# Kernel optimization log

Measured on AMD Instinct MI355X. Metric: run time of the kernel, lower is better.

## Reference

```python
import jax, jax.numpy as jnp
import numpy as np

N = 50000      # nodes
E = 600000     # edges
D = 128        # num_features == hidden_dim
H = 1          # heads (only runnable config of this module)
C = 128        # per-head channels
L = 2          # num_layers
G = 64         # graphs in batch
NC = 10        # num_classes


def setup_inputs() -> dict:
    key = jax.random.key(0)
    ks = jax.random.split(key, 12)
    s = 1.0 / np.sqrt(D)
    inp = {
        "x": jax.random.normal(ks[0], (N, D), jnp.float32),
        "edge_index": jax.random.randint(ks[1], (2, E), 0, N),
        "batch": jnp.sort(jax.random.randint(ks[2], (N,), 0, G)),
        # per-layer TransformerConv params (stacked over layers)
        "Wq": jax.random.normal(ks[3], (L, D, H * C), jnp.float32) * s,
        "bq": jax.random.normal(ks[4], (L, H * C), jnp.float32) * 0.01,
        "Wk": jax.random.normal(ks[5], (L, D, H * C), jnp.float32) * s,
        "bk": jax.random.normal(ks[6], (L, H * C), jnp.float32) * 0.01,
        "Wv": jax.random.normal(ks[7], (L, D, H * C), jnp.float32) * s,
        "bv": jax.random.normal(ks[8], (L, H * C), jnp.float32) * 0.01,
        "Ws": jax.random.normal(ks[9], (L, D, H * C), jnp.float32) * s,  # lin_skip (root weight)
        "bs": jax.random.normal(ks[10], (L, H * C), jnp.float32) * 0.01,
        "W_fc": jax.random.normal(ks[11], (H * C, NC), jnp.float32) * (1.0 / np.sqrt(H * C)),
        "b_fc": jnp.zeros((NC,), jnp.float32),
    }
    return inp


def _transformer_conv(x, src, dst, wq, bq, wk, bk, wv, bv, ws, bs):
    n = x.shape[0]
    q = (x @ wq + bq).reshape(n, H, C)
    k = (x @ wk + bk).reshape(n, H, C)
    v = (x @ wv + bv).reshape(n, H, C)
    # edge-wise gather: query from dst (x_i), key/value from src (x_j)
    score = (q[dst] * k[src]).sum(-1) / jnp.sqrt(jnp.float32(C))  # [E, H]
    # segment softmax over incoming edges of each dst node
    m = jax.ops.segment_max(score, dst, num_segments=n)           # [N, H]
    ex = jnp.exp(score - m[dst])
    den = jax.ops.segment_sum(ex, dst, num_segments=n)
    alpha = ex / den[dst]                                         # [E, H]
    agg = jax.ops.segment_sum(alpha[..., None] * v[src], dst, num_segments=n)
    return agg.reshape(n, H * C) + x @ ws + bs                    # concat heads + skip


def reference(x, edge_index, batch, Wq, bq, Wk, bk, Wv, bv, Ws, bs, W_fc, b_fc):
    src, dst = edge_index[0], edge_index[1]
    h = x
    for l in range(L):
        h = jax.nn.relu(_transformer_conv(h, src, dst, Wq[l], bq[l], Wk[l], bk[l],
                                          Wv[l], bv[l], Ws[l], bs[l]))
    # global mean pool per graph
    sums = jax.ops.segment_sum(h, batch, num_segments=G)
    cnts = jax.ops.segment_sum(jnp.ones((h.shape[0],), h.dtype), batch, num_segments=G)
    pooled = sums / jnp.maximum(cnts, 1.0)[:, None]
    logits = pooled @ W_fc + b_fc
    return jax.nn.log_softmax(logits, axis=1)
```

## Files before the change

kernel.cpp:

```cpp
#include <hip/hip_runtime.h>
#include <math.h>

#define NN 50000
#define EE 600000
#define DD 128
#define GG 64
#define NCLS 10
#define PCHUNK 128
#define NTILE (NN / 16)
#define NBUK 196
#define BSTRIDE 4096
#define EPB ((EE + 255) / 256)

typedef __attribute__((ext_vector_type(8))) __bf16 bf16x8;
typedef __attribute__((ext_vector_type(8))) unsigned short u16x8;
typedef __attribute__((ext_vector_type(4))) float f32x4;
typedef __attribute__((ext_vector_type(2))) float f32x2;

__device__ __forceinline__ unsigned short f2bf(float f) {
    unsigned int u = __float_as_uint(f);
    u += 0x7fff + ((u >> 16) & 1);
    return (unsigned short)(u >> 16);
}

__device__ __forceinline__ float bf2f(unsigned short h) {
    return __uint_as_float(((unsigned int)h) << 16);
}

__device__ __forceinline__ float lo16(unsigned int u) { return __uint_as_float(u << 16); }
__device__ __forceinline__ float hi16(unsigned int u) { return __uint_as_float(u & 0xffff0000u); }


__global__ __launch_bounds__(256) void prep_kernel(
    const float* __restrict__ wq, const float* __restrict__ wk,
    const float* __restrict__ wv, const float* __restrict__ ws,
    unsigned short* __restrict__ wt,
    int* __restrict__ bucketcnt, float* __restrict__ gsum) {
    int tid = blockIdx.x * 256 + threadIdx.x;
    int TOT = gridDim.x * 256;
    if (tid < 256) bucketcnt[tid] = 0;
    for (int i = tid; i < GG * DD + GG; i += TOT) gsum[i] = 0.f;
    for (int i = tid; i < 2 * 4 * 16384; i += TOT) {
        int k = i & 127;
        int n = (i >> 7) & 127;
        int lm = i >> 14;
        int l = lm >> 2, m = lm & 3;
        const float* w = (m == 0) ? wq : (m == 1) ? wk : (m == 2) ? wv : ws;
        wt[i] = f2bf(w[l * 16384 + k * 128 + n]);
    }
}


__global__ __launch_bounds__(1024) void bucket_kernel(
    const int* __restrict__ src, const int* __restrict__ dst,
    int* __restrict__ bucketcnt, int2* __restrict__ bedge) {
    __shared__ int hist[256];
    __shared__ int base[256];
    int t = threadIdx.x;
    if (t < 256) hist[t] = 0;
    __syncthreads();
    int e0 = blockIdx.x * EPB;
    int eend = min(e0 + EPB, EE);

    int b0 = -1, b1 = -1, b2 = -1;
    int sl0 = 0, sl1 = 0, sl2 = 0;
    int s0 = 0, s1 = 0, s2 = 0, d0 = 0, d1 = 0, d2 = 0;
    int i = e0 + t;
    if (i < eend) { d0 = dst[i]; s0 = src[i]; b0 = d0 >> 8; sl0 = atomicAdd(&hist[b0], 1); }
    i += 1024;
    if (i < eend) { d1 = dst[i]; s1 = src[i]; b1 = d1 >> 8; sl1 = atomicAdd(&hist[b1], 1); }
    i += 1024;
    if (i < eend) { d2 = dst[i]; s2 = src[i]; b2 = d2 >> 8; sl2 = atomicAdd(&hist[b2], 1); }
    __syncthreads();

    if (t < 256) {
        int h = hist[t];
        base[t] = h ? atomicAdd(&bucketcnt[t], h) : 0;
    }
    __syncthreads();

    if (b0 >= 0) bedge[b0 * BSTRIDE + base[b0] + sl0] = make_int2(s0, d0);
    if (b1 >= 0) bedge[b1 * BSTRIDE + base[b1] + sl1] = make_int2(s1, d1);
    if (b2 >= 0) bedge[b2 * BSTRIDE + base[b2] + sl2] = make_int2(s2, d2);
}


__global__ __launch_bounds__(1024) void bsort_kernel(
    const int* __restrict__ bucketcnt, const int2* __restrict__ bedge,
    int* __restrict__ indptr, int* __restrict__ esrc) {
    __shared__ int buf[256];
    __shared__ int cur[256];
    int b = blockIdx.x;
    int t = threadIdx.x;

    if (t < 256) buf[t] = (t < NBUK) ? bucketcnt[t] : 0;
    __syncthreads();
    if (t < 64) {
        int carry = 0;
        #pragma unroll
        for (int c = 0; c < 4; ++c) {
            int v = buf[c * 64 + t];
            int x = v;
            #pragma unroll
            for (int off = 1; off < 64; off <<= 1) {
                int y = __shfl_up(x, off);
                if (t >= off) x += y;
            }
            cur[c * 64 + t] = carry + x - v;
            carry += __shfl(x, 63);
        }
    }
    __syncthreads();
    int count = buf[b];
    int bstart = cur[b];
    int node0 = b << 8;
    int nn = min(256, NN - node0);
    if (b == 0 && t == 0) indptr[NN] = EE;
    __syncthreads();
    if (t < 256) buf[t] = 0;
    __syncthreads();

    const int2* be = bedge + (size_t)b * BSTRIDE;
    for (int i2 = t; i2 < count; i2 += 1024)
        atomicAdd(&buf[be[i2].y - node0], 1);
    __syncthreads();

    if (t < 64) {
        int carry = 0;
        #pragma unroll
        for (int c = 0; c < 4; ++c) {
            int v = buf[c * 64 + t];
            int x = v;
            #pragma unroll
            for (int off = 1; off < 64; off <<= 1) {
                int y = __shfl_up(x, off);
                if (t >= off) x += y;
            }
            cur[c * 64 + t] = carry + x - v;
            carry += __shfl(x, 63);
        }
    }
    __syncthreads();
    if (t < nn) indptr[node0 + t] = bstart + cur[t];
    __syncthreads();

    for (int i2 = t; i2 < count; i2 += 1024) {
        int2 e = be[i2];
        int slot = atomicAdd(&cur[e.y - node0], 1);
        esrc[bstart + slot] = e.x;
    }
}


template <bool IN_BF16>
__global__ __launch_bounds__(256, 4) void gemm_mfma(
    const void* __restrict__ xin,
    const unsigned short* __restrict__ wt,
    const float* __restrict__ bq, const float* __restrict__ bk,
    const float* __restrict__ bv, const float* __restrict__ bs,
    unsigned short* __restrict__ qb, unsigned short* __restrict__ kvb,
    unsigned short* __restrict__ sb) {
    int gw = blockIdx.x * 4 + (threadIdx.x >> 6);
    int lane = threadIdx.x & 63;
    int mat = (gw >> 1) & 3;
    int ch = gw & 1;
    int wseq = gw >> 3;
    int lr = lane & 15, quad = lane >> 4;

    const unsigned short* wm_ = wt + mat * 16384;
    const float* bias = (mat == 0) ? bq : (mat == 1) ? bk : (mat == 2) ? bv : bs;
    unsigned short* outp; int ostride, ooff;
    if (mat == 0)      { outp = qb;  ostride = 128; ooff = 0; }
    else if (mat == 1) { outp = kvb; ostride = 256; ooff = 0; }
    else if (mat == 2) { outp = kvb; ostride = 256; ooff = 128; }
    else               { outp = sb;  ostride = 128; ooff = 0; }

    bf16x8 bfr[4][4];
    #pragma unroll
    for (int ks = 0; ks < 4; ++ks)
        #pragma unroll
        for (int tn = 0; tn < 4; ++tn)
            bfr[ks][tn] = *(const bf16x8*)(wm_ + (ch * 64 + tn * 16 + lr) * 128
                                               + ks * 32 + quad * 8);
    float bcol[4];
    #pragma unroll
    for (int tn = 0; tn < 4; ++tn) bcol[tn] = bias[ch * 64 + tn * 16 + lr];

    for (int tile = wseq; tile < NTILE; tile += 256) {
        int row0 = tile * 16;
        bf16x8 af[4];
        #pragma unroll
        for (int ks = 0; ks < 4; ++ks) {
            if (IN_BF16) {
                af[ks] = *(const bf16x8*)((const unsigned short*)xin
                             + (size_t)(row0 + lr) * DD + ks * 32 + quad * 8);
            } else {
                const float* p = (const float*)xin
                                 + (size_t)(row0 + lr) * DD + ks * 32 + quad * 8;
                float4 f0 = *(const float4*)p;
                float4 f1 = *(const float4*)(p + 4);
                u16x8 a8;
                a8[0] = f2bf(f0.x); a8[1] = f2bf(f0.y); a8[2] = f2bf(f0.z); a8[3] = f2bf(f0.w);
                a8[4] = f2bf(f1.x); a8[5] = f2bf(f1.y); a8[6] = f2bf(f1.z); a8[7] = f2bf(f1.w);
                af[ks] = *(bf16x8*)&a8;
            }
        }

        f32x4 acc[4];
        #pragma unroll
        for (int tn = 0; tn < 4; ++tn) acc[tn] = (f32x4){0.f, 0.f, 0.f, 0.f};
        #pragma unroll
        for (int ks = 0; ks < 4; ++ks)
            #pragma unroll
            for (int tn = 0; tn < 4; ++tn)
                acc[tn] = __builtin_amdgcn_mfma_f32_16x16x32_bf16(
                    af[ks], bfr[ks][tn], acc[tn], 0, 0, 0);

        #pragma unroll
        for (int tn = 0; tn < 4; ++tn) {
            int col = ch * 64 + tn * 16 + lr;
            int nb = row0 + quad * 4;
            #pragma unroll
            for (int r = 0; r < 4; ++r)
                outp[(size_t)(nb + r) * ostride + ooff + col] = f2bf(acc[tn][r] + bcol[tn]);
        }
    }
}


__global__ __launch_bounds__(256) void kv8_kernel(
    const unsigned short* __restrict__ kvb, unsigned char* __restrict__ kv8) {
    int idx = blockIdx.x * 256 + threadIdx.x;
    int node = idx >> 4, j = idx & 15;
    const unsigned short* base = kvb + (size_t)node * 256;
    uint4 kin = *(const uint4*)(base + j * 8);
    uint4 vin = *(const uint4*)(base + 128 + j * 8);
    unsigned int w0 = __builtin_amdgcn_cvt_pk_fp8_f32(lo16(kin.x), hi16(kin.x), 0, false);
    w0 = __builtin_amdgcn_cvt_pk_fp8_f32(lo16(kin.y), hi16(kin.y), w0, true);
    unsigned int w1 = __builtin_amdgcn_cvt_pk_fp8_f32(lo16(kin.z), hi16(kin.z), 0, false);
    w1 = __builtin_amdgcn_cvt_pk_fp8_f32(lo16(kin.w), hi16(kin.w), w1, true);
    unsigned int w2 = __builtin_amdgcn_cvt_pk_fp8_f32(lo16(vin.x), hi16(vin.x), 0, false);
    w2 = __builtin_amdgcn_cvt_pk_fp8_f32(lo16(vin.y), hi16(vin.y), w2, true);
    unsigned int w3 = __builtin_amdgcn_cvt_pk_fp8_f32(lo16(vin.z), hi16(vin.z), 0, false);
    w3 = __builtin_amdgcn_cvt_pk_fp8_f32(lo16(vin.w), hi16(vin.w), w3, true);
    *(uint4*)(kv8 + (size_t)idx * 16) = make_uint4(w0, w1, w2, w3);
}


__global__ __launch_bounds__(256) void attn_kernel(
    const unsigned short* __restrict__ qb, const unsigned char* __restrict__ kv8,
    const unsigned short* __restrict__ sb,
    const int* __restrict__ indptr, const int* __restrict__ esrc,
    unsigned short* __restrict__ hout, int n) {
    int node = (int)((blockIdx.x * blockDim.x + threadIdx.x) >> 6);
    int lane = threadIdx.x & 63;
    if (node >= n) return;
    int g = lane >> 4, j = lane & 15;

    u16x8 q8 = *(const u16x8*)(qb + (size_t)node * DD + j * 8);
    float qf[8];
    #pragma unroll
    for (int c = 0; c < 8; ++c) qf[c] = bf2f(q8[c]);

    int beg = indptr[node], end = indptr[node + 1];

    float m = -3.0e38f, den = 0.f;
    float acc[8];
    #pragma unroll
    for (int c = 0; c < 8; ++c) acc[c] = 0.f;

    int e = beg + g;
    if (e < end) {
        int sidx = esrc[e];
        int en = e + 4;
        int sn = (en < end) ? esrc[en] : 0;
        uint4 kv = *(const uint4*)(kv8 + (size_t)sidx * 256 + j * 16);
        for (;;) {
            bool haven = en < end;
            int en2 = en + 4;
            int sn2 = (en2 < end) ? esrc[en2] : 0;
            uint4 kvn;
            if (haven)
                kvn = *(const uint4*)(kv8 + (size_t)sn * 256 + j * 16);
            f32x2 k01 = __builtin_amdgcn_cvt_pk_f32_fp8(kv.x, false);
            f32x2 k23 = __builtin_amdgcn_cvt_pk_f32_fp8(kv.x, true);
            f32x2 k45 = __builtin_amdgcn_cvt_pk_f32_fp8(kv.y, false);
            f32x2 k67 = __builtin_amdgcn_cvt_pk_f32_fp8(kv.y, true);
            float p_;
            p_ = qf[0] * k01.x;
            p_ = fmaf(qf[1], k01.y, p_);
            p_ = fmaf(qf[2], k23.x, p_);
            p_ = fmaf(qf[3], k23.y, p_);
            p_ = fmaf(qf[4], k45.x, p_);
            p_ = fmaf(qf[5], k45.y, p_);
            p_ = fmaf(qf[6], k67.x, p_);
            p_ = fmaf(qf[7], k67.y, p_);
            p_ += __shfl_xor(p_, 8);
            p_ += __shfl_xor(p_, 4);
            p_ += __shfl_xor(p_, 2);
            p_ += __shfl_xor(p_, 1);
            float score = p_ * 0.088388347648318447f;
            float mn = fmaxf(m, score);
            float scale = __expf(m - mn);
            float pe = __expf(score - mn);
            den = den * scale + pe;
            f32x2 v01 = __builtin_amdgcn_cvt_pk_f32_fp8(kv.z, false);
            f32x2 v23 = __builtin_amdgcn_cvt_pk_f32_fp8(kv.z, true);
            f32x2 v45 = __builtin_amdgcn_cvt_pk_f32_fp8(kv.w, false);
            f32x2 v67 = __builtin_amdgcn_cvt_pk_f32_fp8(kv.w, true);
            acc[0] = fmaf(acc[0], scale, pe * v01.x);
            acc[1] = fmaf(acc[1], scale, pe * v01.y);
            acc[2] = fmaf(acc[2], scale, pe * v23.x);
            acc[3] = fmaf(acc[3], scale, pe * v23.y);
            acc[4] = fmaf(acc[4], scale, pe * v45.x);
            acc[5] = fmaf(acc[5], scale, pe * v45.y);
            acc[6] = fmaf(acc[6], scale, pe * v67.x);
            acc[7] = fmaf(acc[7], scale, pe * v67.y);
            m = mn;
            if (!haven) break;
            en = en2; sn = sn2; kv = kvn;
        }
    }

    float mo = __shfl_xor(m, 16);
    float m2 = fmaxf(m, mo);
    mo = __shfl_xor(m2, 32);
    float mf = fmaxf(m2, mo);
    float sc = __expf(m - mf);
    den *= sc;
    den += __shfl_xor(den, 16);
    den += __shfl_xor(den, 32);
    #pragma unroll
    for (int c = 0; c < 8; ++c) {
        float a = acc[c] * sc;
        a += __shfl_xor(a, 16);
        a += __shfl_xor(a, 32);
        acc[c] = a;
    }
    float inv = den > 0.f ? 1.0f / den : 0.f;
    if (g == 0) {
        u16x8 s8 = *(const u16x8*)(sb + (size_t)node * DD + j * 8);
        u16x8 o8;
        #pragma unroll
        for (int c = 0; c < 8; ++c)
            o8[c] = f2bf(fmaxf(fmaf(acc[c], inv, bf2f(s8[c])), 0.f));
        *(u16x8*)(hout + (size_t)node * DD + j * 8) = o8;
    }
}


__global__ __launch_bounds__(128) void pool_kernel(const unsigned short* __restrict__ h,
                                                   const int* __restrict__ batch,
                                                   float* __restrict__ gsum,
                                                   float* __restrict__ gcnt, int n) {
    __shared__ int bsh[PCHUNK];
    int t = threadIdx.x;
    int node0 = blockIdx.x * PCHUNK;
    int nnodes = min(PCHUNK, n - node0);
    if (t < nnodes) bsh[t] = batch[node0 + t];
    __syncthreads();

    int cur = bsh[0];
    float acc = 0.f;
    int cnt = 0;
    for (int j = 0; j < nnodes; ++j) {
        int g = bsh[j];
        float val = bf2f(h[(size_t)(node0 + j) * DD + t]);
        if (g != cur) {
            atomicAdd(&gsum[cur * DD + t], acc);
            if (t == 0) atomicAdd(&gcnt[cur], (float)cnt);
            acc = 0.f; cnt = 0; cur = g;
        }
        acc += val; ++cnt;
    }
    if (cnt > 0) {
        atomicAdd(&gsum[cur * DD + t], acc);
        if (t == 0) atomicAdd(&gcnt[cur], (float)cnt);
    }
}


__global__ __launch_bounds__(64) void head_kernel(
    const float* __restrict__ gsum, const float* __restrict__ gcnt,
    const float* __restrict__ wfc, const float* __restrict__ bfc,
    float* __restrict__ out) {
    int g = blockIdx.x;
    int lane = threadIdx.x;
    float cnt = fmaxf(gcnt[g], 1.0f);
    float inv = 1.0f / cnt;
    float p0 = gsum[g * DD + lane] * inv;
    float p1 = gsum[g * DD + lane + 64] * inv;
    __shared__ float logits[NCLS];
    for (int c = 0; c < NCLS; ++c) {
        float partial = p0 * wfc[lane * NCLS + c] + p1 * wfc[(lane + 64) * NCLS + c];
        partial += __shfl_xor(partial, 32);
        partial += __shfl_xor(partial, 16);
        partial += __shfl_xor(partial, 8);
        partial += __shfl_xor(partial, 4);
        partial += __shfl_xor(partial, 2);
        partial += __shfl_xor(partial, 1);
        if (lane == 0) logits[c] = partial + bfc[c];
    }
    __syncthreads();
    if (lane == 0) {
        float mx = logits[0];
        for (int c = 1; c < NCLS; ++c) mx = fmaxf(mx, logits[c]);
        float sum = 0.f;
        for (int c = 0; c < NCLS; ++c) sum += expf(logits[c] - mx);
        float lse = mx + logf(sum);
        for (int c = 0; c < NCLS; ++c) out[g * NCLS + c] = logits[c] - lse;
    }
}


extern "C" void kernel_launch(void* const* d_in, const int* in_sizes, int n_in,
                              void* d_out, int out_size, void* d_ws, size_t ws_size,
                              hipStream_t stream) {
    const float* x     = (const float*)d_in[0];
    const int*   ei    = (const int*)d_in[1];
    const int*   batch = (const int*)d_in[2];
    const float* Wq = (const float*)d_in[3];
    const float* bq = (const float*)d_in[4];
    const float* Wk = (const float*)d_in[5];
    const float* bk = (const float*)d_in[6];
    const float* Wv = (const float*)d_in[7];
    const float* bv = (const float*)d_in[8];
    const float* Ws = (const float*)d_in[9];
    const float* bs = (const float*)d_in[10];
    const float* Wfc = (const float*)d_in[11];
    const float* bfc = (const float*)d_in[12];
    float* out = (float*)d_out;

    const size_t ND = (size_t)NN * DD;
    unsigned short* hbuf = (unsigned short*)d_ws;
    unsigned short* qb  = hbuf + ND;
    unsigned short* sb  = qb + ND;
    unsigned short* kvb = sb + ND;
    unsigned short* wt  = kvb + 2 * ND;
    unsigned char*  kv8 = (unsigned char*)(wt + 2 * 4 * 16384);
    int* bucketcnt = (int*)(kv8 + (size_t)NN * 256);
    int* indptr    = bucketcnt + 256;
    int* esrc      = indptr + NN + 1;
    int2* bedge    = (int2*)(esrc + EE);
    float* gsum = (float*)(bedge + NBUK * BSTRIDE);
    float* gcnt = gsum + GG * DD;

    const int* src = ei;
    const int* dst = ei + EE;

    prep_kernel<<<256, 256, 0, stream>>>(Wq, Wk, Wv, Ws, wt, bucketcnt, gsum);
    bucket_kernel<<<256, 1024, 0, stream>>>(src, dst, bucketcnt, bedge);
    bsort_kernel<<<NBUK, 1024, 0, stream>>>(bucketcnt, bedge, indptr, esrc);

    for (int l = 0; l < 2; ++l) {
        size_t bo = (size_t)l * DD;
        const unsigned short* wtl = wt + (size_t)l * 4 * 16384;
        if (l == 0)
            gemm_mfma<false><<<512, 256, 0, stream>>>(
                (const void*)x, wtl, bq + bo, bk + bo, bv + bo, bs + bo,
                qb, kvb, sb);
        else
            gemm_mfma<true><<<512, 256, 0, stream>>>(
                (const void*)hbuf, wtl, bq + bo, bk + bo, bv + bo, bs + bo,
                qb, kvb, sb);
        kv8_kernel<<<(NN * 16) / 256, 256, 0, stream>>>(kvb, kv8);
        attn_kernel<<<(NN + 3) / 4, 256, 0, stream>>>(
            qb, kv8, sb, indptr, esrc, hbuf, NN);
    }

    pool_kernel<<<(NN + PCHUNK - 1) / PCHUNK, 128, 0, stream>>>(hbuf, batch, gsum, gcnt, NN);
    head_kernel<<<GG, 64, 0, stream>>>(gsum, gcnt, Wfc, bfc, out);
}
```

Baseline: 272.2 us.

## Software-pipeline GEMM tile loads, stage output via LDS, narrow per-wave column span

The projection GEMM now gives each wave 32 output columns instead of 64 and doubles the grid so the wave count rises. Input rows for the next tile are prefetched into registers while the current tile's MFMAs run. Results are staged through shared memory so each lane writes a 16-byte vector instead of scattered 2-byte stores. The cost is more redundant reads of input rows, since four waves per matrix now load the same tile, plus extra LDS traffic and register pressure from the prefetch buffer.

```diff
diff --git a/kernel.cpp b/kernel.cpp
--- a/kernel.cpp
+++ b/kernel.cpp
@@ -1,5 +1,6 @@
 #include <hip/hip_runtime.h>
 #include <math.h>
+#include <type_traits>
 
 #define NN 50000
 #define EE 600000
@@ -160,11 +161,15 @@
     const float* __restrict__ bv, const float* __restrict__ bs,
     unsigned short* __restrict__ qb, unsigned short* __restrict__ kvb,
     unsigned short* __restrict__ sb) {
-    int gw = blockIdx.x * 4 + (threadIdx.x >> 6);
+    __shared__ __align__(16) unsigned short stg[4][16][56];
+
+    int wid = threadIdx.x >> 6;
     int lane = threadIdx.x & 63;
-    int mat = (gw >> 1) & 3;
-    int ch = gw & 1;
-    int wseq = gw >> 3;
+    int gw = blockIdx.x * 4 + wid;
+    int ch2 = gw & 3;
+    int mat = (gw >> 2) & 3;
+    int wseq = gw >> 4;
+    int wstride = gridDim.x >> 2;
     int lr = lane & 15, quad = lane >> 4;
 
     const unsigned short* wm_ = wt + mat * 16384;
@@ -175,55 +180,84 @@
     else if (mat == 2) { outp = kvb; ostride = 256; ooff = 128; }
     else               { outp = sb;  ostride = 128; ooff = 0; }
 
-    bf16x8 bfr[4][4];
+    bf16x8 bfr[4][2];
     #pragma unroll
     for (int ks = 0; ks < 4; ++ks)
         #pragma unroll
-        for (int tn = 0; tn < 4; ++tn)
-            bfr[ks][tn] = *(const bf16x8*)(wm_ + (ch * 64 + tn * 16 + lr) * 128
+        for (int tn = 0; tn < 2; ++tn)
+            bfr[ks][tn] = *(const bf16x8*)(wm_ + (ch2 * 32 + tn * 16 + lr) * 128
                                                + ks * 32 + quad * 8);
-    float bcol[4];
+    float bcol[2];
     #pragma unroll
-    for (int tn = 0; tn < 4; ++tn) bcol[tn] = bias[ch * 64 + tn * 16 + lr];
-
-    for (int tile = wseq; tile < NTILE; tile += 256) {
-        int row0 = tile * 16;
+    for (int tn = 0; tn < 2; ++tn) bcol[tn] = bias[ch2 * 32 + tn * 16 + lr];
+
+    constexpr int NLD = IN_BF16 ? 4 : 8;
+    using LT = typename std::conditional<IN_BF16, bf16x8, float4>::type;
+    LT buf[NLD];
+
+    auto load_tile = [&](int t) {
+        int row0 = t * 16;
+        if constexpr (IN_BF16) {
+            const unsigned short* p = (const unsigned short*)xin
+                                      + (size_t)(row0 + lr) * DD + quad * 8;
+            #pragma unroll
+            for (int ks = 0; ks < 4; ++ks)
+                buf[ks] = *(const bf16x8*)(p + ks * 32);
+        } else {
+            const float* p = (const float*)xin + (size_t)(row0 + lr) * DD + quad * 8;
+            #pragma unroll
+            for (int ks = 0; ks < 4; ++ks) {
+                buf[2 * ks]     = *(const float4*)(p + ks * 32);
+                buf[2 * ks + 1] = *(const float4*)(p + ks * 32 + 4);
+            }
+        }
+    };
+
+    int tile = wseq;
+    load_tile(tile);
+    while (true) {
         bf16x8 af[4];
-        #pragma unroll
-        for (int ks = 0; ks < 4; ++ks) {
-            if (IN_BF16) {
-                af[ks] = *(const bf16x8*)((const unsigned short*)xin
-                             + (size_t)(row0 + lr) * DD + ks * 32 + quad * 8);
-            } else {
-                const float* p = (const float*)xin
-                                 + (size_t)(row0 + lr) * DD + ks * 32 + quad * 8;
-                float4 f0 = *(const float4*)p;
-                float4 f1 = *(const float4*)(p + 4);
+        if constexpr (IN_BF16) {
+            #pragma unroll
+            for (int ks = 0; ks < 4; ++ks) af[ks] = buf[ks];
+        } else {
+            #pragma unroll
+            for (int ks = 0; ks < 4; ++ks) {
+                float4 f0 = buf[2 * ks], f1 = buf[2 * ks + 1];
                 u16x8 a8;
                 a8[0] = f2bf(f0.x); a8[1] = f2bf(f0.y); a8[2] = f2bf(f0.z); a8[3] = f2bf(f0.w);
                 a8[4] = f2bf(f1.x); a8[5] = f2bf(f1.y); a8[6] = f2bf(f1.z); a8[7] = f2bf(f1.w);
                 af[ks] = *(bf16x8*)&a8;
             }
         }
-
-        f32x4 acc[4];
-        #pragma unroll
-        for (int tn = 0; tn < 4; ++tn) acc[tn] = (f32x4){0.f, 0.f, 0.f, 0.f};
+        int row0 = tile * 16;
+        int nxt = tile + wstride;
+        bool have = nxt < NTILE;
+        if (have) load_tile(nxt);
+
+        f32x4 acc[2];
+        acc[0] = (f32x4){0.f, 0.f, 0.f, 0.f};
+        acc[1] = (f32x4){0.f, 0.f, 0.f, 0.f};
         #pragma unroll
         for (int ks = 0; ks < 4; ++ks)
             #pragma unroll
-            for (int tn = 0; tn < 4; ++tn)
+            for (int tn = 0; tn < 2; ++tn)
                 acc[tn] = __builtin_amdgcn_mfma_f32_16x16x32_bf16(
                     af[ks], bfr[ks][tn], acc[tn], 0, 0, 0);
 
         #pragma unroll
-        for (int tn = 0; tn < 4; ++tn) {
-            int col = ch * 64 + tn * 16 + lr;
-            int nb = row0 + quad * 4;
+        for (int tn = 0; tn < 2; ++tn)
             #pragma unroll
             for (int r = 0; r < 4; ++r)
-                outp[(size_t)(nb + r) * ostride + ooff + col] = f2bf(acc[tn][r] + bcol[tn]);
-        }
+                stg[wid][quad * 4 + r][tn * 16 + lr] = f2bf(acc[tn][r] + bcol[tn]);
+        {
+            int rr = lane >> 2;
+            int c8 = (lane & 3) * 8;
+            u16x8 o = *(const u16x8*)&stg[wid][rr][c8];
+            *(u16x8*)(outp + (size_t)(row0 + rr) * ostride + ooff + ch2 * 32 + c8) = o;
+        }
+        if (!have) break;
+        tile = nxt;
     }
 }
 
@@ -456,11 +490,11 @@
         size_t bo = (size_t)l * DD;
         const unsigned short* wtl = wt + (size_t)l * 4 * 16384;
         if (l == 0)
-            gemm_mfma<false><<<512, 256, 0, stream>>>(
+            gemm_mfma<false><<<1024, 256, 0, stream>>>(
                 (const void*)x, wtl, bq + bo, bk + bo, bv + bo, bs + bo,
                 qb, kvb, sb);
         else
-            gemm_mfma<true><<<512, 256, 0, stream>>>(
+            gemm_mfma<true><<<1024, 256, 0, stream>>>(
                 (const void*)hbuf, wtl, bq + bo, bk + bo, bv + bo, bs + bo,
                 qb, kvb, sb);
         kv8_kernel<<<(NN * 16) / 256, 256, 0, stream>>>(kvb, kv8);
```

Result: slower. 294.6 us (+8.2%).

## Fuse fp8 K/V conversion into GEMM epilogue via LDS staging

Applied to the files above, without the earlier changes.

The GEMM now launches one 512-thread block per 16-row tile. Its eight waves compute all four projections for that tile and stage the bf16 results in shared memory. From there the block writes Q and skip as coalesced 16-byte stores, and converts K/V straight to fp8 into the kv8 buffer. This removes the separate kv8 kernel and the bf16 K/V intermediate round-trip through global memory. In exchange, each block reloads the full weight fragments into registers for a single tile, where the old persistent loop amortized that load over many tiles, and it adds a block-wide barrier.

```diff
diff --git a/kernel.cpp b/kernel.cpp
--- a/kernel.cpp
+++ b/kernel.cpp
@@ -153,27 +153,24 @@
 
 
 template <bool IN_BF16>
-__global__ __launch_bounds__(256, 4) void gemm_mfma(
+__global__ __launch_bounds__(512, 4) void gemm_mfma(
     const void* __restrict__ xin,
     const unsigned short* __restrict__ wt,
     const float* __restrict__ bq, const float* __restrict__ bk,
     const float* __restrict__ bv, const float* __restrict__ bs,
-    unsigned short* __restrict__ qb, unsigned short* __restrict__ kvb,
-    unsigned short* __restrict__ sb) {
-    int gw = blockIdx.x * 4 + (threadIdx.x >> 6);
+    unsigned short* __restrict__ qb, unsigned short* __restrict__ sb,
+    unsigned char* __restrict__ kv8) {
+    __shared__ __align__(16) unsigned short stg[4][16][136];
+
+    int wid = threadIdx.x >> 6;
     int lane = threadIdx.x & 63;
-    int mat = (gw >> 1) & 3;
-    int ch = gw & 1;
-    int wseq = gw >> 3;
+    int mat = wid >> 1;
+    int ch = wid & 1;
     int lr = lane & 15, quad = lane >> 4;
+    int row0 = blockIdx.x * 16;
 
     const unsigned short* wm_ = wt + mat * 16384;
     const float* bias = (mat == 0) ? bq : (mat == 1) ? bk : (mat == 2) ? bv : bs;
-    unsigned short* outp; int ostride, ooff;
-    if (mat == 0)      { outp = qb;  ostride = 128; ooff = 0; }
-    else if (mat == 1) { outp = kvb; ostride = 256; ooff = 0; }
-    else if (mat == 2) { outp = kvb; ostride = 256; ooff = 128; }
-    else               { outp = sb;  ostride = 128; ooff = 0; }
 
     bf16x8 bfr[4][4];
     #pragma unroll
@@ -186,64 +183,61 @@
     #pragma unroll
     for (int tn = 0; tn < 4; ++tn) bcol[tn] = bias[ch * 64 + tn * 16 + lr];
 
-    for (int tile = wseq; tile < NTILE; tile += 256) {
-        int row0 = tile * 16;
-        bf16x8 af[4];
-        #pragma unroll
-        for (int ks = 0; ks < 4; ++ks) {
-            if (IN_BF16) {
-                af[ks] = *(const bf16x8*)((const unsigned short*)xin
-                             + (size_t)(row0 + lr) * DD + ks * 32 + quad * 8);
-            } else {
-                const float* p = (const float*)xin
-                                 + (size_t)(row0 + lr) * DD + ks * 32 + quad * 8;
-                float4 f0 = *(const float4*)p;
-                float4 f1 = *(const float4*)(p + 4);
-                u16x8 a8;
-                a8[0] = f2bf(f0.x); a8[1] = f2bf(f0.y); a8[2] = f2bf(f0.z); a8[3] = f2bf(f0.w);
-                a8[4] = f2bf(f1.x); a8[5] = f2bf(f1.y); a8[6] = f2bf(f1.z); a8[7] = f2bf(f1.w);
-                af[ks] = *(bf16x8*)&a8;
-            }
+    bf16x8 af[4];
+    #pragma unroll
+    for (int ks = 0; ks < 4; ++ks) {
+        if (IN_BF16) {
+            af[ks] = *(const bf16x8*)((const unsigned short*)xin
+                         + (size_t)(row0 + lr) * DD + ks * 32 + quad * 8);
+        } else {
+            const float* p = (const float*)xin
+                             + (size_t)(row0 + lr) * DD + ks * 32 + quad * 8;
+            float4 f0 = *(const float4*)p;
+            float4 f1 = *(const float4*)(p + 4);
+            u16x8 a8;
+            a8[0] = f2bf(f0.x); a8[1] = f2bf(f0.y); a8[2] = f2bf(f0.z); a8[3] = f2bf(f0.w);
+            a8[4] = f2bf(f1.x); a8[5] = f2bf(f1.y); a8[6] = f2bf(f1.z); a8[7] = f2bf(f1.w);
+            af[ks] = *(bf16x8*)&a8;
         }
-
-        f32x4 acc[4];
-        #pragma unroll
-        for (int tn = 0; tn < 4; ++tn) acc[tn] = (f32x4){0.f, 0.f, 0.f, 0.f};
-        #pragma unroll
-        for (int ks = 0; ks < 4; ++ks)
-            #pragma unroll
-            for (int tn = 0; tn < 4; ++tn)
-                acc[tn] = __builtin_amdgcn_mfma_f32_16x16x32_bf16(
-                    af[ks], bfr[ks][tn], acc[tn], 0, 0, 0);
-
-        #pragma unroll
-        for (int tn = 0; tn < 4; ++tn) {
-            int col = ch * 64 + tn * 16 + lr;
-            int nb = row0 + quad * 4;
-            #pragma unroll
-            for (int r = 0; r < 4; ++r)
-                outp[(size_t)(nb + r) * ostride + ooff + col] = f2bf(acc[tn][r] + bcol[tn]);
-        }
-    }
-}
-
-
-__global__ __launch_bounds__(256) void kv8_kernel(
-    const unsigned short* __restrict__ kvb, unsigned char* __restrict__ kv8) {
-    int idx = blockIdx.x * 256 + threadIdx.x;
-    int node = idx >> 4, j = idx & 15;
-    const unsigned short* base = kvb + (size_t)node * 256;
-    uint4 kin = *(const uint4*)(base + j * 8);
-    uint4 vin = *(const uint4*)(base + 128 + j * 8);
-    unsigned int w0 = __builtin_amdgcn_cvt_pk_fp8_f32(lo16(kin.x), hi16(kin.x), 0, false);
-    w0 = __builtin_amdgcn_cvt_pk_fp8_f32(lo16(kin.y), hi16(kin.y), w0, true);
-    unsigned int w1 = __builtin_amdgcn_cvt_pk_fp8_f32(lo16(kin.z), hi16(kin.z), 0, false);
-    w1 = __builtin_amdgcn_cvt_pk_fp8_f32(lo16(kin.w), hi16(kin.w), w1, true);
-    unsigned int w2 = __builtin_amdgcn_cvt_pk_fp8_f32(lo16(vin.x), hi16(vin.x), 0, false);
-    w2 = __builtin_amdgcn_cvt_pk_fp8_f32(lo16(vin.y), hi16(vin.y), w2, true);
-    unsigned int w3 = __builtin_amdgcn_cvt_pk_fp8_f32(lo16(vin.z), hi16(vin.z), 0, false);
-    w3 = __builtin_amdgcn_cvt_pk_fp8_f32(lo16(vin.w), hi16(vin.w), w3, true);
-    *(uint4*)(kv8 + (size_t)idx * 16) = make_uint4(w0, w1, w2, w3);
+    }
+
+    f32x4 acc[4];
+    #pragma unroll
+    for (int tn = 0; tn < 4; ++tn) acc[tn] = (f32x4){0.f, 0.f, 0.f, 0.f};
+    #pragma unroll
+    for (int ks = 0; ks < 4; ++ks)
+        #pragma unroll
+        for (int tn = 0; tn < 4; ++tn)
+            acc[tn] = __builtin_amdgcn_mfma_f32_16x16x32_bf16(
+                af[ks], bfr[ks][tn], acc[tn], 0, 0, 0);
+
+    #pragma unroll
+    for (int tn = 0; tn < 4; ++tn)
+        #pragma unroll
+        for (int r = 0; r < 4; ++r)
+            stg[mat][quad * 4 + r][ch * 64 + tn * 16 + lr] = f2bf(acc[tn][r] + bcol[tn]);
+    __syncthreads();
+
+    int t = threadIdx.x;
+    {
+        int sel = t >> 8;
+        int t2 = t & 255;
+        int rr = t2 >> 4, c8 = (t2 & 15) * 8;
+        uint4 vv = *(const uint4*)&stg[sel ? 3 : 0][rr][c8];
+        unsigned short* op = sel ? sb : qb;
+        *(uint4*)(op + (size_t)(row0 + rr) * 128 + c8) = vv;
+    }
+    {
+        int rr = t >> 5, j5 = t & 31;
+        int half = j5 & 1;
+        int c = (j5 >> 1) * 8;
+        uint4 vv = *(const uint4*)&stg[1 + half][rr][c];
+        unsigned int w0 = __builtin_amdgcn_cvt_pk_fp8_f32(lo16(vv.x), hi16(vv.x), 0, false);
+        w0 = __builtin_amdgcn_cvt_pk_fp8_f32(lo16(vv.y), hi16(vv.y), w0, true);
+        unsigned int w1 = __builtin_amdgcn_cvt_pk_fp8_f32(lo16(vv.z), hi16(vv.z), 0, false);
+        w1 = __builtin_amdgcn_cvt_pk_fp8_f32(lo16(vv.w), hi16(vv.w), w1, true);
+        *(uint2*)(kv8 + (size_t)(row0 + rr) * 256 + j5 * 8) = make_uint2(w0, w1);
+    }
 }
 
 
@@ -435,8 +429,7 @@
     unsigned short* hbuf = (unsigned short*)d_ws;
     unsigned short* qb  = hbuf + ND;
     unsigned short* sb  = qb + ND;
-    unsigned short* kvb = sb + ND;
-    unsigned short* wt  = kvb + 2 * ND;
+    unsigned short* wt  = sb + ND;
     unsigned char*  kv8 = (unsigned char*)(wt + 2 * 4 * 16384);
     int* bucketcnt = (int*)(kv8 + (size_t)NN * 256);
     int* indptr    = bucketcnt + 256;
@@ -456,14 +449,13 @@
         size_t bo = (size_t)l * DD;
         const unsigned short* wtl = wt + (size_t)l * 4 * 16384;
         if (l == 0)
-            gemm_mfma<false><<<512, 256, 0, stream>>>(
+            gemm_mfma<false><<<NTILE, 512, 0, stream>>>(
                 (const void*)x, wtl, bq + bo, bk + bo, bv + bo, bs + bo,
-                qb, kvb, sb);
+                qb, sb, kv8);
         else
-            gemm_mfma<true><<<512, 256, 0, stream>>>(
+            gemm_mfma<true><<<NTILE, 512, 0, stream>>>(
                 (const void*)hbuf, wtl, bq + bo, bk + bo, bv + bo, bs + bo,
-                qb, kvb, sb);
-        kv8_kernel<<<(NN * 16) / 256, 256, 0, stream>>>(kvb, kv8);
+                qb, sb, kv8);
         attn_kernel<<<(NN + 3) / 4, 256, 0, stream>>>(
             qb, kv8, sb, indptr, esrc, hbuf, NN);
     }
```

Measured after the change: 336.1 us. +23.5%, slower.
